# Performance work log

Hardware: AMD Instinct MI355X
Metric: run time of the kernel (lower is better)

## Reference

```python
import jax, jax.numpy as jnp
import numpy as np

D_MODEL, D_STATE, D_CONV, EXPAND = 1024, 16, 4, 2
D_INNER = D_MODEL * EXPAND
B, T = 1, 2048
EPS = 1e-5


def setup_inputs() -> dict:
    key = jax.random.key(0)
    ks = jax.random.split(key, 8)
    x = jax.random.normal(ks[0], (B, T, D_MODEL), dtype=jnp.float32)
    W_in = jax.random.normal(ks[1], (D_MODEL, 2 * D_INNER), dtype=jnp.float32) * 0.02
    conv_w = jax.random.normal(ks[2], (D_INNER, D_CONV), dtype=jnp.float32) * 0.2
    conv_b = jax.random.normal(ks[3], (D_INNER,), dtype=jnp.float32) * 0.02
    W_x = jax.random.normal(ks[4], (D_INNER, 2 * D_STATE + 1), dtype=jnp.float32) * 0.02
    W_dt = jax.random.normal(ks[5], (1, D_INNER), dtype=jnp.float32) * 0.5
    b_dt = jax.random.uniform(ks[6], (D_INNER,), dtype=jnp.float32, minval=-0.001, maxval=0.001)
    A_log = jnp.broadcast_to(jnp.log(jnp.arange(1, D_STATE + 1, dtype=jnp.float32))[None, :], (D_INNER, D_STATE))
    Dparam = jnp.ones((D_INNER,), dtype=jnp.float32)
    W_out = jax.random.normal(ks[7], (D_INNER, D_MODEL), dtype=jnp.float32) * 0.02
    ln_g = jnp.ones((D_MODEL,), dtype=jnp.float32)
    ln_b = jnp.zeros((D_MODEL,), dtype=jnp.float32)
    return {"x": x, "W_in": W_in, "conv_w": conv_w, "conv_b": conv_b, "W_x": W_x,
            "W_dt": W_dt, "b_dt": b_dt, "A_log": A_log, "D": Dparam,
            "W_out": W_out, "ln_g": ln_g, "ln_b": ln_b}


def _silu(v):
    return v * jax.nn.sigmoid(v)


def _layernorm(v, g, b):
    mu = jnp.mean(v, axis=-1, keepdims=True)
    var = jnp.mean((v - mu) ** 2, axis=-1, keepdims=True)
    return (v - mu) * jax.lax.rsqrt(var + EPS) * g + b


def _causal_depthwise_conv(xp, conv_w, conv_b):
    # xp: (B, T, D_INNER) -> (B, D_INNER, T) with left pad of D_CONV-1
    xc = jnp.swapaxes(xp, 1, 2)
    xc = jnp.pad(xc, ((0, 0), (0, 0), (D_CONV - 1, 0)))
    w = conv_w[:, None, :]  # (O=D_INNER, I/groups=1, K)
    out = jax.lax.conv_general_dilated(
        xc, w, window_strides=(1,), padding='VALID',
        dimension_numbers=('NCH', 'OIH', 'NCH'), feature_group_count=D_INNER)
    return jnp.swapaxes(out + conv_b[None, :, None], 1, 2)  # (B, T, D_INNER)


def reference(x, W_in, conv_w, conv_b, W_x, W_dt, b_dt, A_log, D, W_out, ln_g, ln_b):
    residual = x
    xn = _layernorm(x, ln_g, ln_b)
    xz = xn @ W_in                      # (B, T, 2*D_INNER)
    x_proj, z = jnp.split(xz, 2, axis=-1)
    x_conv = _silu(_causal_depthwise_conv(x_proj, conv_w, conv_b))  # (B, T, D_INNER)

    ssm = x_conv @ W_x                  # (B, T, 1 + 2*D_STATE)
    dt_raw = ssm[..., :1]
    Bp = ssm[..., 1:1 + D_STATE]        # (B, T, D_STATE)
    Cp = ssm[..., 1 + D_STATE:]         # (B, T, D_STATE)
    dt = jax.nn.softplus(dt_raw @ W_dt + b_dt)  # (B, T, D_INNER)

    A = -jnp.exp(A_log)                 # (D_INNER, D_STATE)
    A_bar = jnp.exp(dt[..., None] * A)                              # (B,T,d,n)
    Bx = dt[..., None] * Bp[:, :, None, :] * x_conv[..., None]      # (B,T,d,n)

    def step(h, inp):
        Ab_t, Bx_t, C_t = inp           # (B,d,n),(B,d,n),(B,n)
        h = Ab_t * h + Bx_t
        y_t = jnp.einsum('bdn,bn->bd', h, C_t)
        return h, y_t

    h0 = jnp.zeros((x.shape[0], D_INNER, D_STATE), dtype=x.dtype)
    _, ys = jax.lax.scan(step, h0, (jnp.swapaxes(A_bar, 0, 1),
                                    jnp.swapaxes(Bx, 0, 1),
                                    jnp.swapaxes(Cp, 0, 1)))
    y = jnp.swapaxes(ys, 0, 1)          # (B, T, D_INNER)

    y = y + x_conv * D
    y = y * _silu(z)
    return y @ W_out + residual
```

## Files before the change

kernel.cpp:

```cpp
#include <hip/hip_runtime.h>
#include <hip/hip_bf16.h>

typedef __hip_bfloat16 bf16;
typedef __attribute__((ext_vector_type(8))) short bf16x8;
typedef __attribute__((ext_vector_type(4))) float f32x4;

#define T_LEN 2048
#define DMODEL 1024
#define DINNER 2048
#define DSTATE 16
#define LN_EPS 1e-5f
#define NCHUNK 128
#define CLEN 16
#define SSTR 64
#define PSEG 131072
#define KSPLIT 8

#define GLOBAL_AS __attribute__((address_space(1)))
#define LDS_AS __attribute__((address_space(3)))

__device__ __forceinline__ void g2l16(void* lds, const void* g) {
    __builtin_amdgcn_global_load_lds((const GLOBAL_AS void*)g, (LDS_AS void*)lds, 16, 0, 0);
}

__device__ __forceinline__ float b2f(short s) {
    return __uint_as_float(((unsigned)(unsigned short)s) << 16);
}

__device__ __forceinline__ unsigned short f2bu(float f) {
    bf16 b = __float2bfloat16(f);
    return *reinterpret_cast<unsigned short*>(&b);
}

#define BG(buf, j) (buf[(j) >> 2][(j) & 3])

__global__ void prep_all(const float* __restrict__ Win, const float* __restrict__ Wout,
                         const float* __restrict__ Wx, const float* __restrict__ x,
                         const float* __restrict__ lng, const float* __restrict__ lnb,
                         bf16* __restrict__ WinT, bf16* __restrict__ WoutT,
                         bf16* __restrict__ WxT, bf16* __restrict__ xn) {
    __shared__ float t[32][33];
    int bid = blockIdx.x, tid = threadIdx.x;
    int tx = tid & 31, ty4 = (tid >> 5) * 4;
    if (bid < 4096) {
        int n0 = (bid & 127) * 32, k0 = (bid >> 7) * 32;
#pragma unroll
        for (int r = 0; r < 4; r++)
            t[ty4 + r][tx] = Win[(size_t)(k0 + ty4 + r) * 4096 + n0 + tx];
        __syncthreads();
#pragma unroll
        for (int r = 0; r < 4; r++)
            WinT[(size_t)(n0 + ty4 + r) * 1024 + k0 + tx] = __float2bfloat16(t[tx][ty4 + r]);
    } else if (bid < 6144) {
        int b = bid - 4096;
        int n0 = (b & 31) * 32, k0 = (b >> 5) * 32;
#pragma unroll
        for (int r = 0; r < 4; r++)
            t[ty4 + r][tx] = Wout[(size_t)(k0 + ty4 + r) * 1024 + n0 + tx];
        __syncthreads();
#pragma unroll
        for (int r = 0; r < 4; r++)
            WoutT[(size_t)(n0 + ty4 + r) * 2048 + k0 + tx] = __float2bfloat16(t[tx][ty4 + r]);
    } else if (bid < 6656) {
        int idx = (bid - 6144) * 256 + tid;
        int n = idx >> 11, k = idx & 2047;
        int j = (n == 0) ? 0 : (n >= 4 && n <= 35) ? n - 3 : -1;
        WxT[idx] = __float2bfloat16(j >= 0 ? Wx[k * 33 + j] : 0.f);
    } else {
        int row = bid - 6656;
        const float* xr = x + (size_t)row * DMODEL;
        float v[4];
        float s = 0.f, q = 0.f;
#pragma unroll
        for (int i = 0; i < 4; i++) {
            v[i] = xr[tid + i * 256];
            s += v[i];
            q += v[i] * v[i];
        }
        __shared__ float sh_s[256], sh_q[256];
        sh_s[tid] = s; sh_q[tid] = q;
        __syncthreads();
        for (int st = 128; st > 0; st >>= 1) {
            if (tid < st) { sh_s[tid] += sh_s[tid + st]; sh_q[tid] += sh_q[tid + st]; }
            __syncthreads();
        }
        float mean = sh_s[0] * (1.f / DMODEL);
        float var  = sh_q[0] * (1.f / DMODEL) - mean * mean;
        float rstd = rsqrtf(var + LN_EPS);
#pragma unroll
        for (int i = 0; i < 4; i++) {
            int c = tid + i * 256;
            xn[(size_t)row * DMODEL + c] =
                __float2bfloat16((v[i] - mean) * rstd * lng[c] + lnb[c]);
        }
    }
}

template <int BM, int BN, int WAVE_M, int WAVE_N, int WRITE_RESID, int OUT_BF16>
__global__ void gemm_mfma(const bf16* __restrict__ A, const bf16* __restrict__ Bt,
                          void* __restrict__ Cv, const float* __restrict__ resid,
                          int M, int N, int Kslice, int lda) {
    constexpr int WMsz = BM / WAVE_M;
    constexpr int WNsz = BN / WAVE_N;
    constexpr int TM = WMsz / 16;
    constexpr int TN = WNsz / 16;
    __shared__ short As[BM * 64];
    __shared__ short Bs[BN * 64];
    int tid = threadIdx.x;
    int lane = tid & 63, wave = tid >> 6;
    int wm = (wave / WAVE_N) * WMsz, wn = (wave % WAVE_N) * WNsz;
    int rowBase = blockIdx.y * BM, colBase = blockIdx.x * BN;
    int kbase = blockIdx.z * Kslice;

    f32x4 acc[TM][TN];
#pragma unroll
    for (int i = 0; i < TM; i++)
#pragma unroll
        for (int j = 0; j < TN; j++) acc[i][j] = f32x4{0.f, 0.f, 0.f, 0.f};

    int srow = tid >> 3;
    int cc = (tid & 7) ^ (srow & 7);
    const int ldsoff = tid * 16;

    for (int k0 = kbase; k0 < kbase + Kslice; k0 += 64) {
#pragma unroll
        for (int j = 0; j < BM / 32; j++)
            g2l16((char*)As + j * 4096 + ldsoff,
                  A + (size_t)(rowBase + j * 32 + srow) * lda + k0 + cc * 8);
#pragma unroll
        for (int j = 0; j < BN / 32; j++)
            g2l16((char*)Bs + j * 4096 + ldsoff,
                  Bt + (size_t)(colBase + j * 32 + srow) * lda + k0 + cc * 8);
        __syncthreads();
#pragma unroll
        for (int ks = 0; ks < 2; ks++) {
            bf16x8 af[TM], bfr[TN];
#pragma unroll
            for (int i = 0; i < TM; i++) {
                int row = wm + i * 16 + (lane & 15);
                int slot = (ks * 4 + (lane >> 4)) ^ (row & 7);
                af[i] = *(const bf16x8*)((const char*)As + row * 128 + slot * 16);
            }
#pragma unroll
            for (int j = 0; j < TN; j++) {
                int row = wn + j * 16 + (lane & 15);
                int slot = (ks * 4 + (lane >> 4)) ^ (row & 7);
                bfr[j] = *(const bf16x8*)((const char*)Bs + row * 128 + slot * 16);
            }
#pragma unroll
            for (int i = 0; i < TM; i++)
#pragma unroll
                for (int j = 0; j < TN; j++)
                    acc[i][j] = __builtin_amdgcn_mfma_f32_16x16x32_bf16(
                        af[i], bfr[j], acc[i][j], 0, 0, 0);
        }
        __syncthreads();
    }
    int rq = lane >> 4, cn = lane & 15;
    float* Cf = (float*)Cv + (size_t)blockIdx.z * M * N;
#pragma unroll
    for (int i = 0; i < TM; i++) {
#pragma unroll
        for (int j = 0; j < TN; j++) {
#pragma unroll
            for (int r = 0; r < 4; r++) {
                size_t row = rowBase + wm + i * 16 + rq * 4 + r;
                int col = colBase + wn + j * 16 + cn;
                float v = acc[i][j][r];
                if (WRITE_RESID) v += resid[row * N + col];
                if (OUT_BF16)
                    ((bf16*)Cv)[row * N + col] = __float2bfloat16(v);
                else
                    Cf[row * N + col] = v;
            }
        }
    }
}

__global__ void conv_silu(const bf16* __restrict__ xz, const float* __restrict__ cw,
                          const float* __restrict__ cb, bf16* __restrict__ xc) {
    int idx = blockIdx.x * 256 + threadIdx.x;
    int t = idx >> 9, d4 = (idx & 511) * 4;
    const f32x4 bv = *(const f32x4*)(cb + d4);
    float acc0 = bv[0], acc1 = bv[1], acc2 = bv[2], acc3 = bv[3];
    const f32x4* cwv = (const f32x4*)(cw + d4 * 4);
    f32x4 w0 = cwv[0], w1 = cwv[1], w2 = cwv[2], w3 = cwv[3];
#pragma unroll
    for (int k = 0; k < 4; k++) {
        int tt = t - 3 + k;
        if (tt >= 0) {
            ushort4 v = *(const ushort4*)((const short*)xz + (size_t)tt * (2 * DINNER) + d4);
            acc0 = fmaf(b2f((short)v.x), w0[k], acc0);
            acc1 = fmaf(b2f((short)v.y), w1[k], acc1);
            acc2 = fmaf(b2f((short)v.z), w2[k], acc2);
            acc3 = fmaf(b2f((short)v.w), w3[k], acc3);
        }
    }
    ushort4 o;
    o.x = f2bu(acc0 / (1.f + __expf(-acc0)));
    o.y = f2bu(acc1 / (1.f + __expf(-acc1)));
    o.z = f2bu(acc2 / (1.f + __expf(-acc2)));
    o.w = f2bu(acc3 / (1.f + __expf(-acc3)));
    *(ushort4*)((short*)xc + (size_t)t * DINNER + d4) = o;
}

__global__ void reduce_parts(const float* __restrict__ parts, float* __restrict__ ssm) {
    int idx = (blockIdx.x * 256 + threadIdx.x) * 4;
    f32x4 s = f32x4{0.f, 0.f, 0.f, 0.f};
#pragma unroll
    for (int k = 0; k < KSPLIT; k++)
        s += *(const f32x4*)(parts + idx + (size_t)k * PSEG);
    *(f32x4*)(ssm + idx) = s;
}

__device__ __forceinline__ float softplus_f(float pre) {
    return (pre > 20.f) ? pre : log1pf(__expf(pre));
}

__device__ __forceinline__ void powtree(float q, float* a) {
    a[0] = q;
    a[1] = q * q;
    a[2] = a[1] * q;
    a[3] = a[1] * a[1];
#pragma unroll
    for (int j = 0; j < 4; j++) a[4 + j] = a[j] * a[3];
#pragma unroll
    for (int j = 0; j < 8; j++) a[8 + j] = a[j] * a[7];
}

__device__ __forceinline__ void ldrow5(f32x4* b, const f32x4* sp) {
#pragma unroll
    for (int k = 0; k < 5; k++) b[k] = sp[k];
}

__device__ __forceinline__ void ldrow8(f32x4* b, const f32x4* sp) {
#pragma unroll
    for (int k = 0; k < 8; k++) b[k] = sp[k];
}

template <int FAST>
__device__ __forceinline__ void p1_step(const f32x4* buf, short xcs, float wdt, float bd,
                                        const float* A, float& Lsum, float* Sv,
                                        float& dtout) {
    float dt = softplus_f(BG(buf, 0) * wdt + bd);
    dtout = dt;
    Lsum += dt;
    float u = dt * b2f(xcs);
    if (FAST) {
        float a[DSTATE];
        powtree(__expf(-dt), a);
#pragma unroll
        for (int n = 0; n < DSTATE; n++)
            Sv[n] = fmaf(a[n], Sv[n], u * BG(buf, 4 + n));
    } else {
#pragma unroll
        for (int n = 0; n < DSTATE; n++)
            Sv[n] = fmaf(__expf(dt * A[n]), Sv[n], u * BG(buf, 4 + n));
    }
}

template <int FAST>
__device__ __forceinline__ void p1_loop(const f32x4* sp, const short* xcp,
                                        float wdt, float bd, const float* A,
                                        float& Lsum, float* Sv, float* dtv) {
    short xcv[CLEN];
#pragma unroll
    for (int i = 0; i < CLEN; i++)
        xcv[i] = xcp[(size_t)i * DINNER];
    f32x4 bA[5], bB[5];
    ldrow5(bA, sp);
#pragma unroll
    for (int i = 0; i < CLEN; i += 2) {
        ldrow5(bB, sp + (i + 1) * 16);
        p1_step<FAST>(bA, xcv[i], wdt, bd, A, Lsum, Sv, dtv[i]);
        ldrow5(bA, sp + (i + 2) * 16);
        p1_step<FAST>(bB, xcv[i + 1], wdt, bd, A, Lsum, Sv, dtv[i + 1]);
    }
}

__global__ void scan_pass1(
        const float* __restrict__ ssm, const bf16* __restrict__ xc,
        const float* __restrict__ Wdt, const float* __restrict__ bdt,
        const float* __restrict__ Alog,
        float* __restrict__ Ld, float* __restrict__ S, float* __restrict__ dtb) {
    int tid = threadIdx.x;
    int d = blockIdx.x * 256 + tid;
    int c = blockIdx.y;
    int t0 = c * CLEN;
    float A[DSTATE];
    bool fast = true;
#pragma unroll
    for (int n = 0; n < DSTATE; n++) {
        A[n] = -__expf(Alog[d * DSTATE + n]);
        fast = fast && (fabsf(A[n] + (float)(n + 1)) < 1e-3f * (n + 1));
    }
    float wdt = Wdt[d], bd = bdt[d];
    float Sv[DSTATE];
#pragma unroll
    for (int n = 0; n < DSTATE; n++) Sv[n] = 0.f;
    float Lsum = 0.f;
    float dtv[CLEN];
    const f32x4* sp = (const f32x4*)(ssm + (size_t)t0 * SSTR);
    const short* xcp = (const short*)xc + (size_t)t0 * DINNER + d;
    if (fast)
        p1_loop<1>(sp, xcp, wdt, bd, A, Lsum, Sv, dtv);
    else
        p1_loop<0>(sp, xcp, wdt, bd, A, Lsum, Sv, dtv);
    float* dtp = dtb + (size_t)t0 * DINNER + d;
#pragma unroll
    for (int i = 0; i < CLEN; i++)
        dtp[(size_t)i * DINNER] = dtv[i];
    Ld[(size_t)c * DINNER + d] = Lsum;
    size_t base = (size_t)c * DINNER * DSTATE + d;
#pragma unroll
    for (int n = 0; n < DSTATE; n++)
        S[base + (size_t)n * DINNER] = Sv[n];
}

#define SEGL (NCHUNK / 4)
__global__ void scan_pass2(const float* __restrict__ Ld, const float* __restrict__ S,
                           const float* __restrict__ Alog, float* __restrict__ Hst) {
    int tx = threadIdx.x & 63, ty = threadIdx.x >> 6;
    int d = blockIdx.x * 64 + tx;
    int n = blockIdx.y;
    float A = -__expf(Alog[d * DSTATE + n]);
    int c0 = ty * SEGL;
    float lv[SEGL], sv[SEGL];
#pragma unroll
    for (int j = 0; j < SEGL; j++) {
        int cc = c0 + j;
        lv[j] = Ld[(size_t)cc * DINNER + d];
        sv[j] = S[(size_t)cc * DINNER * DSTATE + (size_t)n * DINNER + d];
    }
    float Lsum = 0.f, Sseg = 0.f;
#pragma unroll
    for (int j = 0; j < SEGL; j++) {
        Sseg = fmaf(__expf(A * lv[j]), Sseg, sv[j]);
        Lsum += lv[j];
    }
    __shared__ float shL[4][64], shS[4][64], shC[4][64];
    shL[ty][tx] = Lsum;
    shS[ty][tx] = Sseg;
    __syncthreads();
    if (ty == 0) {
        float car = 0.f;
        shC[0][tx] = 0.f;
#pragma unroll
        for (int s = 0; s < 3; s++) {
            car = fmaf(__expf(A * shL[s][tx]), car, shS[s][tx]);
            shC[s + 1][tx] = car;
        }
    }
    __syncthreads();
    float H = shC[ty][tx];
#pragma unroll
    for (int j = 0; j < SEGL; j++) {
        size_t o = (size_t)(c0 + j) * DINNER * DSTATE + (size_t)n * DINNER + d;
        Hst[o] = H;
        H = fmaf(__expf(A * lv[j]), H, sv[j]);
    }
}

template <int FAST>
__device__ __forceinline__ void p3_step(const f32x4* buf, float dt, float q,
                                        short xcs, short zs,
                                        float Dd, const float* A,
                                        float* h, bf16* outp) {
    float xcf = b2f(xcs);
    float u = dt * xcf;
    float y;
    if (FAST) {
        float a[DSTATE];
        powtree(q, a);
        float y0 = 0.f, y1 = 0.f, y2 = 0.f, y3 = 0.f;
#pragma unroll
        for (int n = 0; n < 4; n++) {
            h[n]      = fmaf(a[n],      h[n],      u * BG(buf, n));
            y0 = fmaf(h[n],      BG(buf, 16 + n), y0);
            h[n + 4]  = fmaf(a[n + 4],  h[n + 4],  u * BG(buf, 4 + n));
            y1 = fmaf(h[n + 4],  BG(buf, 20 + n), y1);
            h[n + 8]  = fmaf(a[n + 8],  h[n + 8],  u * BG(buf, 8 + n));
            y2 = fmaf(h[n + 8],  BG(buf, 24 + n), y2);
            h[n + 12] = fmaf(a[n + 12], h[n + 12], u * BG(buf, 12 + n));
            y3 = fmaf(h[n + 12], BG(buf, 28 + n), y3);
        }
        y = (y0 + y1) + (y2 + y3);
    } else {
        y = 0.f;
#pragma unroll
        for (int n = 0; n < DSTATE; n++) {
            float a = __expf(dt * A[n]);
            h[n] = fmaf(a, h[n], u * BG(buf, n));
            y = fmaf(h[n], BG(buf, 16 + n), y);
        }
    }
    float z = b2f(zs);
    float sz = z / (1.f + __expf(-z));
    *outp = __float2bfloat16(fmaf(xcf, Dd, y) * sz);
}

template <int FAST>
__device__ __forceinline__ void p3_loop(const f32x4* sp8, const float* dtp,
                                        const short* xcp, const short* zp,
                                        float Dd, const float* A,
                                        float* h, bf16* yp) {
    float dtv[CLEN], qv[CLEN];
    short xcv[CLEN], zv[CLEN];
#pragma unroll
    for (int i = 0; i < CLEN; i++) {
        dtv[i] = dtp[(size_t)i * DINNER];
        xcv[i] = xcp[(size_t)i * DINNER];
        zv[i]  = zp[(size_t)i * 2 * DINNER];
    }
#pragma unroll
    for (int i = 0; i < CLEN; i++)
        qv[i] = FAST ? __expf(-dtv[i]) : 0.f;
    f32x4 bA[8], bB[8];
    ldrow8(bA, sp8);
#pragma unroll
    for (int i = 0; i < CLEN; i += 2) {
        ldrow8(bB, sp8 + (i + 1) * 16);
        p3_step<FAST>(bA, dtv[i], qv[i], xcv[i], zv[i], Dd, A, h,
                      yp + (size_t)i * DINNER);
        ldrow8(bA, sp8 + (i + 2) * 16);
        p3_step<FAST>(bB, dtv[i + 1], qv[i + 1], xcv[i + 1], zv[i + 1], Dd, A, h,
                      yp + (size_t)(i + 1) * DINNER);
    }
}

__global__ void scan_pass3(
        const float* __restrict__ ssm, const float* __restrict__ dtb,
        const bf16* __restrict__ xc, const bf16* __restrict__ xz,
        const float* __restrict__ Alog, const float* __restrict__ Dp,
        const float* __restrict__ Hst, bf16* __restrict__ yf) {
    int tid = threadIdx.x;
    int d = blockIdx.x * 256 + tid;
    int c = blockIdx.y;
    int t0 = c * CLEN;
    float A[DSTATE], h[DSTATE];
    bool fast = true;
    size_t base = (size_t)c * DINNER * DSTATE + d;
#pragma unroll
    for (int n = 0; n < DSTATE; n++) {
        A[n] = -__expf(Alog[d * DSTATE + n]);
        fast = fast && (fabsf(A[n] + (float)(n + 1)) < 1e-3f * (n + 1));
        h[n] = Hst[base + (size_t)n * DINNER];
    }
    float Dd = Dp[d];
    const f32x4* sp8 = (const f32x4*)(ssm + (size_t)t0 * SSTR) + 1;
    const float* dtp = dtb + (size_t)t0 * DINNER + d;
    const short* xcp = (const short*)xc + (size_t)t0 * DINNER + d;
    const short* zp  = (const short*)xz + (size_t)t0 * (2 * DINNER) + DINNER + d;
    bf16* yp = yf + (size_t)t0 * DINNER + d;
    if (fast)
        p3_loop<1>(sp8, dtp, xcp, zp, Dd, A, h, yp);
    else
        p3_loop<0>(sp8, dtp, xcp, zp, Dd, A, h, yp);
}

extern "C" void kernel_launch(void* const* d_in, const int* in_sizes, int n_in,
                              void* d_out, int out_size, void* d_ws, size_t ws_size,
                              hipStream_t stream) {
    const float* x     = (const float*)d_in[0];
    const float* W_in  = (const float*)d_in[1];
    const float* convw = (const float*)d_in[2];
    const float* convb = (const float*)d_in[3];
    const float* W_x   = (const float*)d_in[4];
    const float* W_dt  = (const float*)d_in[5];
    const float* b_dt  = (const float*)d_in[6];
    const float* A_log = (const float*)d_in[7];
    const float* Dp    = (const float*)d_in[8];
    const float* W_out = (const float*)d_in[9];
    const float* ln_g  = (const float*)d_in[10];
    const float* ln_b  = (const float*)d_in[11];
    float* out = (float*)d_out;

    char* wsb = (char*)d_ws;
    bf16*  xn    = (bf16*)(wsb);
    bf16*  WinT  = (bf16*)(wsb + (4ull  << 20));
    bf16*  WoutT = (bf16*)(wsb + (12ull << 20));
    bf16*  WxT   = (bf16*)(wsb + (16ull << 20));
    bf16*  xz    = (bf16*)(wsb + (17ull << 20));
    bf16*  xc    = (bf16*)(wsb + (33ull << 20));
    float* parts = (float*)(wsb + (41ull << 20));
    float* Ld    = (float*)(wsb + (45ull << 20));
    float* Hst   = (float*)(wsb + (46ull << 20));
    float* S     = (float*)(wsb + (62ull << 20));
    bf16*  yf    = (bf16*)(wsb + (78ull << 20));
    float* ssm   = (float*)(wsb + (86ull << 20));
    float* dtb   = (float*)(wsb + (88ull << 20));

    prep_all<<<8704, 256, 0, stream>>>(W_in, W_out, W_x, x, ln_g, ln_b,
                                       WinT, WoutT, WxT, xn);

    gemm_mfma<128, 128, 2, 2, 0, 1><<<dim3(4096 / 128, 2048 / 128), 256, 0, stream>>>(
        xn, WinT, xz, nullptr, 2048, 4096, 1024, 1024);

    conv_silu<<<(T_LEN * DINNER / 4) / 256, 256, 0, stream>>>(xz, convw, convb, xc);

    gemm_mfma<32, 64, 2, 2, 0, 0><<<dim3(1, 2048 / 32, KSPLIT), 256, 0, stream>>>(
        xc, WxT, parts, nullptr, 2048, 64, 2048 / KSPLIT, 2048);

    reduce_parts<<<(T_LEN * SSTR / 4) / 256, 256, 0, stream>>>(parts, ssm);

    scan_pass1<<<dim3(DINNER / 256, NCHUNK), 256, 0, stream>>>(
        ssm, xc, W_dt, b_dt, A_log, Ld, S, dtb);
    scan_pass2<<<dim3(DINNER / 64, DSTATE), 256, 0, stream>>>(Ld, S, A_log, Hst);
    scan_pass3<<<dim3(DINNER / 256, NCHUNK), 256, 0, stream>>>(
        ssm, dtb, xc, xz, A_log, Dp, Hst, yf);

    gemm_mfma<64, 64, 2, 2, 1, 0><<<dim3(1024 / 64, 2048 / 64), 256, 0, stream>>>(
        yf, WoutT, out, x, 2048, 1024, 2048, 2048);
}
```

Baseline: 221.5 us.

## Compute local scan outputs in pass1 and apply carry-in correction in pass3

Pass1 now produces each chunk's zero-initialised local output and the cumulative dt sum per timestep. Pass3 then skips re-running the recurrence and only adds the carried-in state contribution, C·exp(A·Lt)·H, to the stored local output. This moves the sequential 16-state recurrence out of pass3 but writes two fp32 T×D buffers instead of one. The W_x split-K factor also drops from 8 to 4, and the workspace offsets are reshuffled to make room.

```diff
diff --git a/kernel.cpp b/kernel.cpp
--- a/kernel.cpp
+++ b/kernel.cpp
@@ -14,7 +14,7 @@
 #define CLEN 16
 #define SSTR 64
 #define PSEG 131072
-#define KSPLIT 8
+#define KSPLIT 4
 
 #define GLOBAL_AS __attribute__((address_space(1)))
 #define LDS_AS __attribute__((address_space(3)))
@@ -228,61 +228,17 @@
     for (int j = 0; j < 8; j++) a[8 + j] = a[j] * a[7];
 }
 
-__device__ __forceinline__ void ldrow5(f32x4* b, const f32x4* sp) {
-#pragma unroll
-    for (int k = 0; k < 5; k++) b[k] = sp[k];
-}
-
-__device__ __forceinline__ void ldrow8(f32x4* b, const f32x4* sp) {
-#pragma unroll
-    for (int k = 0; k < 8; k++) b[k] = sp[k];
-}
-
-template <int FAST>
-__device__ __forceinline__ void p1_step(const f32x4* buf, short xcs, float wdt, float bd,
-                                        const float* A, float& Lsum, float* Sv,
-                                        float& dtout) {
-    float dt = softplus_f(BG(buf, 0) * wdt + bd);
-    dtout = dt;
-    Lsum += dt;
-    float u = dt * b2f(xcs);
-    if (FAST) {
-        float a[DSTATE];
-        powtree(__expf(-dt), a);
-#pragma unroll
-        for (int n = 0; n < DSTATE; n++)
-            Sv[n] = fmaf(a[n], Sv[n], u * BG(buf, 4 + n));
-    } else {
-#pragma unroll
-        for (int n = 0; n < DSTATE; n++)
-            Sv[n] = fmaf(__expf(dt * A[n]), Sv[n], u * BG(buf, 4 + n));
-    }
-}
-
-template <int FAST>
-__device__ __forceinline__ void p1_loop(const f32x4* sp, const short* xcp,
-                                        float wdt, float bd, const float* A,
-                                        float& Lsum, float* Sv, float* dtv) {
-    short xcv[CLEN];
-#pragma unroll
-    for (int i = 0; i < CLEN; i++)
-        xcv[i] = xcp[(size_t)i * DINNER];
-    f32x4 bA[5], bB[5];
-    ldrow5(bA, sp);
-#pragma unroll
-    for (int i = 0; i < CLEN; i += 2) {
-        ldrow5(bB, sp + (i + 1) * 16);
-        p1_step<FAST>(bA, xcv[i], wdt, bd, A, Lsum, Sv, dtv[i]);
-        ldrow5(bA, sp + (i + 2) * 16);
-        p1_step<FAST>(bB, xcv[i + 1], wdt, bd, A, Lsum, Sv, dtv[i + 1]);
-    }
+__device__ __forceinline__ void ldrow9(f32x4* b, const f32x4* sp) {
+#pragma unroll
+    for (int k = 0; k < 9; k++) b[k] = sp[k];
 }
 
 __global__ void scan_pass1(
         const float* __restrict__ ssm, const bf16* __restrict__ xc,
         const float* __restrict__ Wdt, const float* __restrict__ bdt,
         const float* __restrict__ Alog,
-        float* __restrict__ Ld, float* __restrict__ S, float* __restrict__ dtb) {
+        float* __restrict__ Ld, float* __restrict__ S,
+        float* __restrict__ Lt, float* __restrict__ yloc) {
     int tid = threadIdx.x;
     int d = blockIdx.x * 256 + tid;
     int c = blockIdx.y;
@@ -299,17 +255,58 @@
 #pragma unroll
     for (int n = 0; n < DSTATE; n++) Sv[n] = 0.f;
     float Lsum = 0.f;
-    float dtv[CLEN];
     const f32x4* sp = (const f32x4*)(ssm + (size_t)t0 * SSTR);
     const short* xcp = (const short*)xc + (size_t)t0 * DINNER + d;
-    if (fast)
-        p1_loop<1>(sp, xcp, wdt, bd, A, Lsum, Sv, dtv);
-    else
-        p1_loop<0>(sp, xcp, wdt, bd, A, Lsum, Sv, dtv);
-    float* dtp = dtb + (size_t)t0 * DINNER + d;
+    short xcv[CLEN];
 #pragma unroll
     for (int i = 0; i < CLEN; i++)
-        dtp[(size_t)i * DINNER] = dtv[i];
+        xcv[i] = xcp[(size_t)i * DINNER];
+    float* Ltp = Lt + (size_t)t0 * DINNER + d;
+    float* ylp = yloc + (size_t)t0 * DINNER + d;
+    if (fast) {
+#pragma unroll
+        for (int i = 0; i < CLEN; i++) {
+            f32x4 buf[9];
+            ldrow9(buf, sp + i * 16);
+            float dt = softplus_f(BG(buf, 0) * wdt + bd);
+            Lsum += dt;
+            float u = dt * b2f(xcv[i]);
+            float a[DSTATE];
+            powtree(__expf(-dt), a);
+            float y0 = 0.f, y1 = 0.f, y2 = 0.f, y3 = 0.f;
+#pragma unroll
+            for (int n = 0; n < 4; n++) {
+                Sv[n]      = fmaf(a[n],      Sv[n],      u * BG(buf, 4 + n));
+                y0 = fmaf(Sv[n],      BG(buf, 20 + n), y0);
+                Sv[n + 4]  = fmaf(a[n + 4],  Sv[n + 4],  u * BG(buf, 8 + n));
+                y1 = fmaf(Sv[n + 4],  BG(buf, 24 + n), y1);
+                Sv[n + 8]  = fmaf(a[n + 8],  Sv[n + 8],  u * BG(buf, 12 + n));
+                y2 = fmaf(Sv[n + 8],  BG(buf, 28 + n), y2);
+                Sv[n + 12] = fmaf(a[n + 12], Sv[n + 12], u * BG(buf, 16 + n));
+                y3 = fmaf(Sv[n + 12], BG(buf, 32 + n), y3);
+            }
+            Ltp[(size_t)i * DINNER] = Lsum;
+            ylp[(size_t)i * DINNER] = (y0 + y1) + (y2 + y3);
+        }
+    } else {
+#pragma unroll
+        for (int i = 0; i < CLEN; i++) {
+            f32x4 buf[9];
+            ldrow9(buf, sp + i * 16);
+            float dt = softplus_f(BG(buf, 0) * wdt + bd);
+            Lsum += dt;
+            float u = dt * b2f(xcv[i]);
+            float y = 0.f;
+#pragma unroll
+            for (int n = 0; n < DSTATE; n++) {
+                float a = __expf(dt * A[n]);
+                Sv[n] = fmaf(a, Sv[n], u * BG(buf, 4 + n));
+                y = fmaf(Sv[n], BG(buf, 20 + n), y);
+            }
+            Ltp[(size_t)i * DINNER] = Lsum;
+            ylp[(size_t)i * DINNER] = y;
+        }
+    }
     Ld[(size_t)c * DINNER + d] = Lsum;
     size_t base = (size_t)c * DINNER * DSTATE + d;
 #pragma unroll
@@ -361,75 +358,9 @@
     }
 }
 
-template <int FAST>
-__device__ __forceinline__ void p3_step(const f32x4* buf, float dt, float q,
-                                        short xcs, short zs,
-                                        float Dd, const float* A,
-                                        float* h, bf16* outp) {
-    float xcf = b2f(xcs);
-    float u = dt * xcf;
-    float y;
-    if (FAST) {
-        float a[DSTATE];
-        powtree(q, a);
-        float y0 = 0.f, y1 = 0.f, y2 = 0.f, y3 = 0.f;
-#pragma unroll
-        for (int n = 0; n < 4; n++) {
-            h[n]      = fmaf(a[n],      h[n],      u * BG(buf, n));
-            y0 = fmaf(h[n],      BG(buf, 16 + n), y0);
-            h[n + 4]  = fmaf(a[n + 4],  h[n + 4],  u * BG(buf, 4 + n));
-            y1 = fmaf(h[n + 4],  BG(buf, 20 + n), y1);
-            h[n + 8]  = fmaf(a[n + 8],  h[n + 8],  u * BG(buf, 8 + n));
-            y2 = fmaf(h[n + 8],  BG(buf, 24 + n), y2);
-            h[n + 12] = fmaf(a[n + 12], h[n + 12], u * BG(buf, 12 + n));
-            y3 = fmaf(h[n + 12], BG(buf, 28 + n), y3);
-        }
-        y = (y0 + y1) + (y2 + y3);
-    } else {
-        y = 0.f;
-#pragma unroll
-        for (int n = 0; n < DSTATE; n++) {
-            float a = __expf(dt * A[n]);
-            h[n] = fmaf(a, h[n], u * BG(buf, n));
-            y = fmaf(h[n], BG(buf, 16 + n), y);
-        }
-    }
-    float z = b2f(zs);
-    float sz = z / (1.f + __expf(-z));
-    *outp = __float2bfloat16(fmaf(xcf, Dd, y) * sz);
-}
-
-template <int FAST>
-__device__ __forceinline__ void p3_loop(const f32x4* sp8, const float* dtp,
-                                        const short* xcp, const short* zp,
-                                        float Dd, const float* A,
-                                        float* h, bf16* yp) {
-    float dtv[CLEN], qv[CLEN];
-    short xcv[CLEN], zv[CLEN];
-#pragma unroll
-    for (int i = 0; i < CLEN; i++) {
-        dtv[i] = dtp[(size_t)i * DINNER];
-        xcv[i] = xcp[(size_t)i * DINNER];
-        zv[i]  = zp[(size_t)i * 2 * DINNER];
-    }
-#pragma unroll
-    for (int i = 0; i < CLEN; i++)
-        qv[i] = FAST ? __expf(-dtv[i]) : 0.f;
-    f32x4 bA[8], bB[8];
-    ldrow8(bA, sp8);
-#pragma unroll
-    for (int i = 0; i < CLEN; i += 2) {
-        ldrow8(bB, sp8 + (i + 1) * 16);
-        p3_step<FAST>(bA, dtv[i], qv[i], xcv[i], zv[i], Dd, A, h,
-                      yp + (size_t)i * DINNER);
-        ldrow8(bA, sp8 + (i + 2) * 16);
-        p3_step<FAST>(bB, dtv[i + 1], qv[i + 1], xcv[i + 1], zv[i + 1], Dd, A, h,
-                      yp + (size_t)(i + 1) * DINNER);
-    }
-}
-
 __global__ void scan_pass3(
-        const float* __restrict__ ssm, const float* __restrict__ dtb,
+        const float* __restrict__ ssm, const float* __restrict__ Lt,
+        const float* __restrict__ yloc,
         const bf16* __restrict__ xc, const bf16* __restrict__ xz,
         const float* __restrict__ Alog, const float* __restrict__ Dp,
         const float* __restrict__ Hst, bf16* __restrict__ yf) {
@@ -437,25 +368,75 @@
     int d = blockIdx.x * 256 + tid;
     int c = blockIdx.y;
     int t0 = c * CLEN;
-    float A[DSTATE], h[DSTATE];
+    float A[DSTATE], H[DSTATE];
     bool fast = true;
     size_t base = (size_t)c * DINNER * DSTATE + d;
 #pragma unroll
     for (int n = 0; n < DSTATE; n++) {
         A[n] = -__expf(Alog[d * DSTATE + n]);
         fast = fast && (fabsf(A[n] + (float)(n + 1)) < 1e-3f * (n + 1));
-        h[n] = Hst[base + (size_t)n * DINNER];
+        H[n] = Hst[base + (size_t)n * DINNER];
     }
     float Dd = Dp[d];
-    const f32x4* sp8 = (const f32x4*)(ssm + (size_t)t0 * SSTR) + 1;
-    const float* dtp = dtb + (size_t)t0 * DINNER + d;
+    const float* Ltp = Lt + (size_t)t0 * DINNER + d;
+    const float* ylp = yloc + (size_t)t0 * DINNER + d;
     const short* xcp = (const short*)xc + (size_t)t0 * DINNER + d;
     const short* zp  = (const short*)xz + (size_t)t0 * (2 * DINNER) + DINNER + d;
     bf16* yp = yf + (size_t)t0 * DINNER + d;
-    if (fast)
-        p3_loop<1>(sp8, dtp, xcp, zp, Dd, A, h, yp);
-    else
-        p3_loop<0>(sp8, dtp, xcp, zp, Dd, A, h, yp);
+    float Ltv[CLEN], ylv[CLEN];
+    short xcv[CLEN], zv[CLEN];
+#pragma unroll
+    for (int i = 0; i < CLEN; i++) {
+        Ltv[i] = Ltp[(size_t)i * DINNER];
+        ylv[i] = ylp[(size_t)i * DINNER];
+        xcv[i] = xcp[(size_t)i * DINNER];
+        zv[i]  = zp[(size_t)i * 2 * DINNER];
+    }
+    if (fast) {
+        float qv[CLEN];
+#pragma unroll
+        for (int i = 0; i < CLEN; i++)
+            qv[i] = __expf(-Ltv[i]);
+#pragma unroll
+        for (int i = 0; i < CLEN; i++) {
+            const f32x4* cp = (const f32x4*)(ssm + (size_t)(t0 + i) * SSTR) + 5;
+            f32x4 cb[4];
+#pragma unroll
+            for (int k = 0; k < 4; k++) cb[k] = cp[k];
+            float a[DSTATE];
+            powtree(qv[i], a);
+            float y0 = 0.f, y1 = 0.f, y2 = 0.f, y3 = 0.f;
+#pragma unroll
+            for (int n = 0; n < 4; n++) {
+                y0 = fmaf(cb[0][n] * a[n],      H[n],      y0);
+                y1 = fmaf(cb[1][n] * a[n + 4],  H[n + 4],  y1);
+                y2 = fmaf(cb[2][n] * a[n + 8],  H[n + 8],  y2);
+                y3 = fmaf(cb[3][n] * a[n + 12], H[n + 12], y3);
+            }
+            float xcf = b2f(xcv[i]);
+            float y = ylv[i] + (y0 + y1) + (y2 + y3);
+            float z = b2f(zv[i]);
+            float sz = z / (1.f + __expf(-z));
+            yp[(size_t)i * DINNER] = __float2bfloat16(fmaf(xcf, Dd, y) * sz);
+        }
+    } else {
+#pragma unroll
+        for (int i = 0; i < CLEN; i++) {
+            const f32x4* cp = (const f32x4*)(ssm + (size_t)(t0 + i) * SSTR) + 5;
+            f32x4 cb[4];
+#pragma unroll
+            for (int k = 0; k < 4; k++) cb[k] = cp[k];
+            float corr = 0.f;
+#pragma unroll
+            for (int n = 0; n < DSTATE; n++)
+                corr = fmaf(cb[n >> 2][n & 3] * __expf(A[n] * Ltv[i]), H[n], corr);
+            float xcf = b2f(xcv[i]);
+            float y = ylv[i] + corr;
+            float z = b2f(zv[i]);
+            float sz = z / (1.f + __expf(-z));
+            yp[(size_t)i * DINNER] = __float2bfloat16(fmaf(xcf, Dd, y) * sz);
+        }
+    }
 }
 
 extern "C" void kernel_launch(void* const* d_in, const int* in_sizes, int n_in,
@@ -483,12 +464,13 @@
     bf16*  xz    = (bf16*)(wsb + (17ull << 20));
     bf16*  xc    = (bf16*)(wsb + (33ull << 20));
     float* parts = (float*)(wsb + (41ull << 20));
-    float* Ld    = (float*)(wsb + (45ull << 20));
-    float* Hst   = (float*)(wsb + (46ull << 20));
-    float* S     = (float*)(wsb + (62ull << 20));
-    bf16*  yf    = (bf16*)(wsb + (78ull << 20));
-    float* ssm   = (float*)(wsb + (86ull << 20));
-    float* dtb   = (float*)(wsb + (88ull << 20));
+    float* Ld    = (float*)(wsb + (43ull << 20));
+    float* Hst   = (float*)(wsb + (44ull << 20));
+    float* S     = (float*)(wsb + (60ull << 20));
+    bf16*  yf    = (bf16*)(wsb + (76ull << 20));
+    float* ssm   = (float*)(wsb + (84ull << 20));
+    float* Lt    = (float*)(wsb + (88ull << 20));
+    float* yloc  = (float*)(wsb + (104ull << 20));
 
     prep_all<<<8704, 256, 0, stream>>>(W_in, W_out, W_x, x, ln_g, ln_b,
                                        WinT, WoutT, WxT, xn);
@@ -504,10 +486,10 @@
     reduce_parts<<<(T_LEN * SSTR / 4) / 256, 256, 0, stream>>>(parts, ssm);
 
     scan_pass1<<<dim3(DINNER / 256, NCHUNK), 256, 0, stream>>>(
-        ssm, xc, W_dt, b_dt, A_log, Ld, S, dtb);
+        ssm, xc, W_dt, b_dt, A_log, Ld, S, Lt, yloc);
     scan_pass2<<<dim3(DINNER / 64, DSTATE), 256, 0, stream>>>(Ld, S, A_log, Hst);
     scan_pass3<<<dim3(DINNER / 256, NCHUNK), 256, 0, stream>>>(
-        ssm, dtb, xc, xz, A_log, Dp, Hst, yf);
+        ssm, Lt, yloc, xc, xz, A_log, Dp, Hst, yf);
 
     gemm_mfma<64, 64, 2, 2, 1, 0><<<dim3(1024 / 64, 2048 / 64), 256, 0, stream>>>(
         yf, WoutT, out, x, 2048, 1024, 2048, 2048);
```

Measured after the change: 223.4 us. No clear change (+0.8%).
